# Kernel tuning notes

Hardware: AMD Instinct MI355X
Metric: run time of the kernel (lower is better)

Reference implementation:

```python
import jax, jax.numpy as jnp
import numpy as np

TOP_K = 2
LB_WEIGHT = 0.01


def _ln(x, g, b, eps=1e-5):
    m = x.mean(-1, keepdims=True)
    v = ((x - m) ** 2).mean(-1, keepdims=True)
    return (x - m) * jax.lax.rsqrt(v + eps) * g + b


def setup_inputs() -> dict:
    key = jax.random.key(0)
    ks = iter(jax.random.split(key, 40))
    B, L, D, CT, CB, E, H = 8, 1024, 1024, 768, 64, 8, 1024
    ID = 3 * D           # concat(id, content_proj, collab_proj)
    GH = max(ID // 2, 128)  # 1536, router gate hidden

    def rn(shape, s=0.02):
        return jax.random.normal(next(ks), shape, jnp.float32) * s

    return {
        "id_emb": rn((B, L, D), 1.0),
        "content_emb": rn((B, L, CT), 1.0),
        "collab_emb": rn((B, L, CB), 1.0),
        "ln_ct_g": jnp.ones(CT), "ln_ct_b": jnp.zeros(CT),
        "ln_cb_g": jnp.ones(CB), "ln_cb_b": jnp.zeros(CB),
        "Wc": rn((CT, D)), "bc": jnp.zeros(D),
        "Wcb": rn((CB, D)), "bcb": jnp.zeros(D),
        "Wg1": rn((ID, GH)), "bg1": jnp.zeros(GH),
        "lng_g": jnp.ones(GH), "lng_b": jnp.zeros(GH),
        "Wg2": rn((GH, GH // 2)), "bg2": jnp.zeros(GH // 2),
        "Wg3": rn((GH // 2, E)), "bg3": jnp.zeros(E),
        "We1": rn((E, ID, H)), "be1": jnp.zeros((E, H)),
        "lne1_g": jnp.ones((E, H)), "lne1_b": jnp.zeros((E, H)),
        "We2": rn((E, H, H // 2)), "be2": jnp.zeros((E, H // 2)),
        "We3": rn((E, H // 2, H // 4)), "be3": jnp.zeros((E, H // 4)),
        "lne3_g": jnp.ones((E, H // 4)), "lne3_b": jnp.zeros((E, H // 4)),
        "Wout": rn((H // 4, D)), "bout": jnp.zeros(D),
        "alpha": jnp.full((1,), 0.1, jnp.float32),
    }


def reference(id_emb, content_emb, collab_emb, ln_ct_g, ln_ct_b, ln_cb_g, ln_cb_b,
              Wc, bc, Wcb, bcb, Wg1, bg1, lng_g, lng_b, Wg2, bg2, Wg3, bg3,
              We1, be1, lne1_g, lne1_b, We2, be2, We3, be3, lne3_g, lne3_b,
              Wout, bout, alpha):
    # --- input normalization + projection to d_model (eval mode: no noise/dropout) ---
    ct = _ln(content_emb, ln_ct_g, ln_ct_b) @ Wc + bc        # (B,L,D)
    cb = _ln(collab_emb, ln_cb_g, ln_cb_b) @ Wcb + bcb       # (B,L,D)
    x = jnp.concatenate([id_emb, ct, cb], axis=-1)           # (B,L,3D)

    # --- router: gate MLP -> softmax -> top-k -> renormalize ---
    g = jax.nn.relu(_ln(x @ Wg1 + bg1, lng_g, lng_b))
    g = jax.nn.relu(g @ Wg2 + bg2)
    probs = jax.nn.softmax(g @ Wg3 + bg3, axis=-1)           # (B,L,E)
    topv, topi = jax.lax.top_k(probs, TOP_K)                 # (B,L,K)
    w = topv / (topv.sum(-1, keepdims=True) + 1e-8)

    # --- experts (dense over E, then gather selected) ---
    h = jax.nn.relu(_ln(jnp.einsum('bld,edh->bleh', x, We1) + be1, lne1_g, lne1_b))
    h = jax.nn.relu(jnp.einsum('bleh,ehm->blem', h, We2) + be2)
    eo = _ln(jnp.einsum('blem,emo->bleo', h, We3) + be3, lne3_g, lne3_b)  # (B,L,E,H/4)
    sel = jnp.take_along_axis(eo, topi[..., None], axis=2)   # (B,L,K,H/4)
    comb = (sel * w[..., None]).sum(axis=2)                  # (B,L,H/4)

    # --- output projection + learnable-alpha residual ---
    fused = id_emb + alpha * (comb @ Wout + bout)            # (B,L,D)

    # --- load balancing loss (importance + entropy terms) ---
    E = probs.shape[-1]
    num_tokens = probs.shape[0] * probs.shape[1]
    counts = jnp.sum(jax.nn.one_hot(topi, E, dtype=jnp.float32), axis=(0, 1, 2))
    f = counts / num_tokens
    P = probs.mean(axis=(0, 1))
    importance = E * (f * P).sum()
    ent = -(P * jnp.log(P + 1e-8)).sum()
    max_ent = jnp.log(jnp.asarray(E, jnp.float32))
    lb_loss = (importance + (max_ent - ent) / max_ent) * LB_WEIGHT
    return fused, lb_loss
```

## Files before the change

kernel.cpp:

```cpp
#include <hip/hip_runtime.h>
#include <hip/hip_bf16.h>

using u16 = unsigned short;
typedef float f32x4 __attribute__((ext_vector_type(4)));
typedef short short8 __attribute__((ext_vector_type(8)));
typedef unsigned short ushort8 __attribute__((ext_vector_type(8)));

typedef __attribute__((address_space(1))) const unsigned int gu32;
typedef __attribute__((address_space(3))) unsigned int lu32;

__device__ __forceinline__ float b2f(u16 u) {
  unsigned v = ((unsigned)u) << 16;
  float f;
  __builtin_memcpy(&f, &v, 4);
  return f;
}
__device__ __forceinline__ u16 f2b(float f) {
  unsigned u;
  __builtin_memcpy(&u, &f, 4);
  unsigned r = (u + 0x7fffu + ((u >> 16) & 1u)) >> 16;
  return (u16)r;
}
__device__ __forceinline__ float ldv(float x) { return x; }
__device__ __forceinline__ float ldv(u16 x) { return b2f(x); }

__device__ __forceinline__ void gl_lds16(const void* g, void* l) {
  __builtin_amdgcn_global_load_lds((gu32*)g, (lu32*)l, 16, 0, 0);
}

template <int D, bool RELU, bool PEREXP, typename TIN>
__global__ void ln_rows(const TIN* __restrict__ in, u16* __restrict__ out,
                        const float* __restrict__ gamma, const float* __restrict__ beta,
                        const int* __restrict__ pairExp, const int* __restrict__ total) {
  constexpr int T = (D >= 256) ? 256 : 64;
  constexpr int VPT = D / T;
  int row = blockIdx.x;
  if constexpr (PEREXP) {
    if (row >= *total) return;
  }
  int t = threadIdx.x;
  const TIN* r = in + (size_t)row * D;
  float vals[VPT];
  float s = 0.f, ss = 0.f;
#pragma unroll
  for (int i = 0; i < VPT; ++i) {
    float v = ldv(r[t + i * T]);
    vals[i] = v;
    s += v;
    ss += v * v;
  }
#pragma unroll
  for (int m = 1; m < 64; m <<= 1) {
    s += __shfl_xor(s, m);
    ss += __shfl_xor(ss, m);
  }
  if constexpr (T == 256) {
    __shared__ float red[8];
    int wave = t >> 6, lane = t & 63;
    if (lane == 0) { red[wave] = s; red[4 + wave] = ss; }
    __syncthreads();
    s = red[0] + red[1] + red[2] + red[3];
    ss = red[4] + red[5] + red[6] + red[7];
  }
  float mean = s / (float)D;
  float var = ss / (float)D - mean * mean;
  var = fmaxf(var, 0.f);
  float rstd = 1.f / sqrtf(var + 1e-5f);
  const float* g = gamma;
  const float* b = beta;
  if constexpr (PEREXP) {
    int e = pairExp[row];
    g += (size_t)e * D;
    b += (size_t)e * D;
  }
  u16* o = out + (size_t)row * D;
#pragma unroll
  for (int i = 0; i < VPT; ++i) {
    int idx = t + i * T;
    float v = (vals[i] - mean) * rstd * g[idx] + b[idx];
    if constexpr (RELU) v = fmaxf(v, 0.f);
    o[idx] = f2b(v);
  }
}

struct PackDesc {
  const float* src;
  u16* dst;
  int K, M, tx, tilesPerMat, base;
};
struct PackTable { PackDesc d[8]; int total; };

__global__ void prepack_all(PackTable tab) {
  int bid = blockIdx.x;
  int w = 0;
#pragma unroll
  for (int i = 1; i < 8; ++i)
    if (bid >= tab.d[i].base) w = i;
  PackDesc pd = tab.d[w];
  int local = bid - pd.base;
  int z = local / pd.tilesPerMat;
  int tl = local % pd.tilesPerMat;
  int m0 = (tl % pd.tx) * 64, k0 = (tl / pd.tx) * 64;
  size_t zo = (size_t)z * pd.K * pd.M;
  const float* ip = pd.src + zo;
  u16* op = pd.dst + zo;

  __shared__ u16 tile[64 * 65];
  int t = threadIdx.x;
#pragma unroll
  for (int h = 0; h < 4; ++h) {
    int u = t + h * 256;
    int kr = u >> 4, mc = (u & 15) * 4;
    f32x4 v = *(const f32x4*)(ip + (size_t)(k0 + kr) * pd.M + m0 + mc);
#pragma unroll
    for (int i = 0; i < 4; ++i) tile[kr * 65 + mc + i] = f2b(v[i]);
  }
  __syncthreads();
#pragma unroll
  for (int h = 0; h < 2; ++h) {
    int u = t + h * 256;
    int mr = u >> 3, kc = (u & 7) * 8;
    ushort8 v;
#pragma unroll
    for (int i = 0; i < 8; ++i) v[i] = tile[(kc + i) * 65 + mr];
    *(ushort8*)(op + (size_t)(m0 + mr) * pd.K + k0 + kc) = v;
  }
}

__global__ void copy_id3(const float* __restrict__ id, u16* __restrict__ xb3) {
  size_t i = ((size_t)blockIdx.x * 256 + threadIdx.x) * 8;
  size_t t = i >> 10, d = i & 1023;
  f32x4 a = *(const f32x4*)(id + i);
  f32x4 b = *(const f32x4*)(id + i + 4);
  ushort8 v;
#pragma unroll
  for (int j = 0; j < 4; ++j) { v[j] = f2b(a[j]); v[j + 4] = f2b(b[j]); }
  *(ushort8*)(xb3 + t * 3072 + d) = v;
}

#define BM 128
#define BN 128
#define BKK 64

template <int EPI, bool EXPERT, bool GATHER>
__global__ __launch_bounds__(256, 3)
void gemm_bf(const u16* __restrict__ A, const u16* __restrict__ Bt,
             const float* __restrict__ bias,
             u16* __restrict__ C, float* __restrict__ Cf,
             int K, int lda, int ldc,
             long strideB, int strideBias,
             const int* __restrict__ offA, const int* __restrict__ pairTok,
             const float* __restrict__ resid, const float* __restrict__ alphaPtr) {
  int rowTile = blockIdx.x * BM;
  int colTile = blockIdx.y * BN;
  if constexpr (EXPERT) {
    if (rowTile >= offA[8]) return;
    int e = 0;
    while (rowTile >= offA[e + 1]) ++e;
    Bt += (size_t)e * strideB;
    bias += (size_t)e * strideBias;
  }

  __shared__ u16 As[BM * BKK];
  __shared__ u16 Bs[BN * BKK];

  int t = threadIdx.x;
  int lane = t & 63;
  int wv = t >> 6;
  int wr = wv >> 1, wc = wv & 1;
  int l15 = lane & 15, l4 = lane >> 4;

  int rowInLane = lane >> 3;
  int colLane = (lane & 7) * 8;
  const u16* aSrc[4];
  const u16* bSrc[4];
  u16* aDst[4];
  u16* bDst[4];
#pragma unroll
  for (int j = 0; j < 4; ++j) {
    int rr = j * 32 + wv * 8 + rowInLane;
    size_t aRow;
    if constexpr (GATHER) {
      aRow = (size_t)pairTok[rowTile + rr] * lda;
    } else {
      aRow = (size_t)(rowTile + rr) * lda;
    }
    aSrc[j] = A + aRow + colLane;
    bSrc[j] = Bt + (size_t)(colTile + rr) * K + colLane;
    aDst[j] = As + (j * 32 + wv * 8) * BKK;
    bDst[j] = Bs + (j * 32 + wv * 8) * BKK;
  }

  f32x4 zero4 = {0.f, 0.f, 0.f, 0.f};
  f32x4 acc[4][4];
#pragma unroll
  for (int m = 0; m < 4; ++m)
#pragma unroll
    for (int n = 0; n < 4; ++n) acc[m][n] = zero4;

  for (int k0 = 0; k0 < K; k0 += BKK) {
    __syncthreads();
#pragma unroll
    for (int j = 0; j < 4; ++j) gl_lds16(aSrc[j] + k0, aDst[j]);
#pragma unroll
    for (int j = 0; j < 4; ++j) gl_lds16(bSrc[j] + k0, bDst[j]);
    asm volatile("s_waitcnt vmcnt(0)" ::: "memory");
    __syncthreads();
    short8 af[4][2];
#pragma unroll
    for (int m = 0; m < 4; ++m)
#pragma unroll
      for (int ks = 0; ks < 2; ++ks)
        af[m][ks] = *(const short8*)&As[(wr * 64 + m * 16 + l15) * BKK + ks * 32 + l4 * 8];
#pragma unroll
    for (int n = 0; n < 4; ++n) {
      short8 bfr[2];
#pragma unroll
      for (int ks = 0; ks < 2; ++ks)
        bfr[ks] = *(const short8*)&Bs[(wc * 64 + n * 16 + l15) * BKK + ks * 32 + l4 * 8];
#pragma unroll
      for (int m = 0; m < 4; ++m)
#pragma unroll
        for (int ks = 0; ks < 2; ++ks)
          acc[m][n] = __builtin_amdgcn_mfma_f32_16x16x32_bf16(af[m][ks], bfr[ks], acc[m][n], 0, 0, 0);
    }
  }

  float alphaV = 0.f;
  if constexpr (EPI == 2) alphaV = alphaPtr[0];
#pragma unroll
  for (int n = 0; n < 4; ++n) {
    int col = colTile + wc * 64 + n * 16 + l15;
    float bv = bias[col];
#pragma unroll
    for (int m = 0; m < 4; ++m) {
      int r2 = rowTile + wr * 64 + m * 16 + l4 * 4;
#pragma unroll
      for (int j = 0; j < 4; ++j) {
        float v = acc[m][n][j] + bv;
        if constexpr (EPI == 1) v = fmaxf(v, 0.f);
        if constexpr (EPI == 2) {
          Cf[(size_t)(r2 + j) * ldc + col] =
              resid[(size_t)(r2 + j) * ldc + col] + alphaV * v;
        } else {
          C[(size_t)(r2 + j) * ldc + col] = f2b(v);
        }
      }
    }
  }
}

__global__ void router_kernel(const u16* __restrict__ g2, const float* __restrict__ Wg3,
                              const float* __restrict__ bg3, float* __restrict__ probs,
                              int* __restrict__ topi, float* __restrict__ wts) {
  int tok = blockIdx.x * 4 + (threadIdx.x >> 6);
  int lane = threadIdx.x & 63;
  const u16* row = g2 + (size_t)tok * 768;
  float acc[8];
#pragma unroll
  for (int e = 0; e < 8; ++e) acc[e] = 0.f;
  for (int j = lane; j < 768; j += 64) {
    float v = b2f(row[j]);
    f32x4 w0 = *(const f32x4*)(Wg3 + (size_t)j * 8);
    f32x4 w1 = *(const f32x4*)(Wg3 + (size_t)j * 8 + 4);
#pragma unroll
    for (int e = 0; e < 4; ++e) { acc[e] += v * w0[e]; acc[e + 4] += v * w1[e]; }
  }
#pragma unroll
  for (int e = 0; e < 8; ++e) {
#pragma unroll
    for (int m = 1; m < 64; m <<= 1) acc[e] += __shfl_xor(acc[e], m);
  }
  if (lane == 0) {
    float lg[8], mx = -3.4e38f;
#pragma unroll
    for (int e = 0; e < 8; ++e) {
      lg[e] = acc[e] + bg3[e];
      mx = fmaxf(mx, lg[e]);
    }
    float p[8], s = 0.f;
#pragma unroll
    for (int e = 0; e < 8; ++e) {
      p[e] = expf(lg[e] - mx);
      s += p[e];
    }
    float inv = 1.f / s;
#pragma unroll
    for (int e = 0; e < 8; ++e) {
      p[e] *= inv;
      probs[(size_t)tok * 8 + e] = p[e];
    }
    int i0 = 0;
    for (int e = 1; e < 8; ++e)
      if (p[e] > p[i0]) i0 = e;
    int i1 = (i0 == 0) ? 1 : 0;
    for (int e = 0; e < 8; ++e)
      if (e != i0 && p[e] > p[i1]) i1 = e;
    float w0 = p[i0], w1 = p[i1];
    float wsum = w0 + w1 + 1e-8f;
    topi[tok * 2] = i0;
    topi[tok * 2 + 1] = i1;
    wts[tok * 2] = w0 / wsum;
    wts[tok * 2 + 1] = w1 / wsum;
  }
}

__global__ void count_kernel(const int* __restrict__ topi, int* __restrict__ cnt,
                             int* __restrict__ offA, int* __restrict__ cursor) {
  __shared__ int c[8];
  int t = threadIdx.x;
  if (t < 8) c[t] = 0;
  __syncthreads();
  for (int i = t; i < 16384; i += 256) atomicAdd(&c[topi[i]], 1);
  __syncthreads();
  if (t == 0) {
    int off = 0;
    for (int e = 0; e < 8; ++e) {
      cnt[e] = c[e];
      offA[e] = off;
      cursor[e] = off;
      off += (c[e] + 127) & ~127;
    }
    offA[8] = off;
  }
}

__global__ void scatter_kernel(const int* __restrict__ topi, int* __restrict__ cursor,
                               int* __restrict__ pairTok, int* __restrict__ pairExp,
                               int* __restrict__ posOf) {
  int i = blockIdx.x * 256 + threadIdx.x;
  int e = topi[i];
  int pos = atomicAdd(&cursor[e], 1);
  pairTok[pos] = i >> 1;
  pairExp[pos] = e;
  posOf[i] = pos;
}

__global__ void padfill_kernel(const int* __restrict__ cnt, const int* __restrict__ offA,
                               int* __restrict__ pairTok, int* __restrict__ pairExp) {
  int e = blockIdx.x;
  int start = offA[e] + cnt[e];
  int end = offA[e + 1];
  for (int i = start + threadIdx.x; i < end; i += 256) {
    pairTok[i] = 0;
    pairExp[i] = e;
  }
}

__global__ void combine_kernel(const u16* __restrict__ eo, const int* __restrict__ posOf,
                               const float* __restrict__ wts, u16* __restrict__ comb) {
  int t = blockIdx.x, d = threadIdx.x;
  int p0 = posOf[t * 2], p1 = posOf[t * 2 + 1];
  float w0 = wts[t * 2], w1 = wts[t * 2 + 1];
  float v = w0 * b2f(eo[(size_t)p0 * 256 + d]) + w1 * b2f(eo[(size_t)p1 * 256 + d]);
  comb[(size_t)t * 256 + d] = f2b(v);
}

__global__ void lbloss_kernel(const float* __restrict__ probs, const int* __restrict__ cnt,
                              float* __restrict__ outp) {
  __shared__ float red[256];
  int t = threadIdx.x;
  float pl[8];
#pragma unroll
  for (int e = 0; e < 8; ++e) pl[e] = 0.f;
  for (int i = t; i < 8192; i += 256) {
#pragma unroll
    for (int e = 0; e < 8; ++e) pl[e] += probs[(size_t)i * 8 + e];
  }
  float P[8];
  for (int e = 0; e < 8; ++e) {
    red[t] = pl[e];
    __syncthreads();
    for (int s = 128; s > 0; s >>= 1) {
      if (t < s) red[t] += red[t + s];
      __syncthreads();
    }
    P[e] = red[0] / 8192.f;
    __syncthreads();
  }
  if (t == 0) {
    float imp = 0.f, ent = 0.f;
    for (int e = 0; e < 8; ++e) {
      float f = (float)cnt[e] / 8192.f;
      imp += f * P[e];
      ent -= P[e] * logf(P[e] + 1e-8f);
    }
    imp *= 8.f;
    float maxent = logf(8.f);
    outp[0] = (imp + (maxent - ent) / maxent) * 0.01f;
  }
}

extern "C" void kernel_launch(void* const* d_in, const int* in_sizes, int n_in,
                              void* d_out, int out_size, void* d_ws, size_t ws_size,
                              hipStream_t stream) {
  const float* id_emb   = (const float*)d_in[0];
  const float* content  = (const float*)d_in[1];
  const float* collab   = (const float*)d_in[2];
  const float* ln_ct_g  = (const float*)d_in[3];
  const float* ln_ct_b  = (const float*)d_in[4];
  const float* ln_cb_g  = (const float*)d_in[5];
  const float* ln_cb_b  = (const float*)d_in[6];
  const float* Wc       = (const float*)d_in[7];
  const float* bc       = (const float*)d_in[8];
  const float* Wcb      = (const float*)d_in[9];
  const float* bcb      = (const float*)d_in[10];
  const float* Wg1      = (const float*)d_in[11];
  const float* bg1      = (const float*)d_in[12];
  const float* lng_g    = (const float*)d_in[13];
  const float* lng_b    = (const float*)d_in[14];
  const float* Wg2      = (const float*)d_in[15];
  const float* bg2      = (const float*)d_in[16];
  const float* Wg3      = (const float*)d_in[17];
  const float* bg3      = (const float*)d_in[18];
  const float* We1      = (const float*)d_in[19];
  const float* be1      = (const float*)d_in[20];
  const float* lne1_g   = (const float*)d_in[21];
  const float* lne1_b   = (const float*)d_in[22];
  const float* We2      = (const float*)d_in[23];
  const float* be2      = (const float*)d_in[24];
  const float* We3      = (const float*)d_in[25];
  const float* be3      = (const float*)d_in[26];
  const float* lne3_g   = (const float*)d_in[27];
  const float* lne3_b   = (const float*)d_in[28];
  const float* Wout     = (const float*)d_in[29];
  const float* bout     = (const float*)d_in[30];
  const float* alpha    = (const float*)d_in[31];
  (void)in_sizes; (void)n_in; (void)out_size; (void)ws_size;

  float* out = (float*)d_out;
  char* ws = (char*)d_ws;
  size_t o = 0;
  auto AL = [&](size_t bytes) {
    size_t r = o;
    o += (bytes + 255) & ~(size_t)255;
    return r;
  };

  u16* WcT   = (u16*)(ws + AL(1024ull * 768 * 2));
  u16* WcbT  = (u16*)(ws + AL(1024ull * 64 * 2));
  u16* Wg1T  = (u16*)(ws + AL(1536ull * 3072 * 2));
  u16* Wg2T  = (u16*)(ws + AL(768ull * 1536 * 2));
  u16* We1T  = (u16*)(ws + AL(8ull * 1024 * 3072 * 2));
  u16* We2T  = (u16*)(ws + AL(8ull * 512 * 1024 * 2));
  u16* We3T  = (u16*)(ws + AL(8ull * 256 * 512 * 2));
  u16* WoutT = (u16*)(ws + AL(1024ull * 256 * 2));
  u16* xb3   = (u16*)(ws + AL(8192ull * 3072 * 2));
  size_t R1  = AL(17408ull * 1024 * 2);
  u16* ct_norm = (u16*)(ws + R1);
  u16* cb_norm = (u16*)(ws + R1 + 8192ull * 768 * 2);
  u16* g1      = (u16*)(ws + R1);
  u16* h1      = (u16*)(ws + R1);
  size_t R2  = AL(17408ull * 512 * 2);
  u16* g2 = (u16*)(ws + R2);
  u16* h2 = (u16*)(ws + R2);
  u16* eo   = (u16*)(ws + AL(17408ull * 256 * 2));
  u16* comb = (u16*)(ws + AL(8192ull * 256 * 2));
  float* probs = (float*)(ws + AL(8192ull * 8 * 4));
  int* topi    = (int*)(ws + AL(8192ull * 2 * 4));
  float* wts   = (float*)(ws + AL(8192ull * 2 * 4));
  int* posOf   = (int*)(ws + AL(8192ull * 2 * 4));
  int* pairTok = (int*)(ws + AL(17408ull * 4));
  int* pairExp = (int*)(ws + AL(17408ull * 4));
  int* cnt     = (int*)(ws + AL(64));
  int* offA    = (int*)(ws + AL(64));
  int* cursor  = (int*)(ws + AL(64));

  PackTable tab;
  auto mk = [](const float* s, u16* d, int K, int M, int z) {
    PackDesc p;
    p.src = s; p.dst = d; p.K = K; p.M = M;
    p.tx = M / 64; p.tilesPerMat = (M / 64) * (K / 64); p.base = 0;
    return p;
  };
  PackDesc descs[8] = {
      mk(Wc, WcT, 768, 1024, 1),    mk(Wcb, WcbT, 64, 1024, 1),
      mk(Wg1, Wg1T, 3072, 1536, 1), mk(Wg2, Wg2T, 1536, 768, 1),
      mk(We1, We1T, 3072, 1024, 8), mk(We2, We2T, 1024, 512, 8),
      mk(We3, We3T, 512, 256, 8),   mk(Wout, WoutT, 256, 1024, 1)};
  int zcount[8] = {1, 1, 1, 1, 8, 8, 8, 1};
  int base = 0;
  for (int i = 0; i < 8; ++i) {
    descs[i].base = base;
    base += descs[i].tilesPerMat * zcount[i];
  }
  for (int i = 0; i < 8; ++i) tab.d[i] = descs[i];
  tab.total = base;
  prepack_all<<<base, 256, 0, stream>>>(tab);

  ln_rows<768, false, false, float><<<8192, 256, 0, stream>>>(content, ct_norm, ln_ct_g, ln_ct_b, nullptr, nullptr);
  ln_rows<64, false, false, float><<<8192, 64, 0, stream>>>(collab, cb_norm, ln_cb_g, ln_cb_b, nullptr, nullptr);
  copy_id3<<<4096, 256, 0, stream>>>(id_emb, xb3);
  gemm_bf<0, false, false><<<dim3(64, 8), 256, 0, stream>>>(
      ct_norm, WcT, bc, xb3 + 1024, nullptr, 768, 768, 3072,
      0, 0, nullptr, nullptr, nullptr, nullptr);
  gemm_bf<0, false, false><<<dim3(64, 8), 256, 0, stream>>>(
      cb_norm, WcbT, bcb, xb3 + 2048, nullptr, 64, 64, 3072,
      0, 0, nullptr, nullptr, nullptr, nullptr);

  gemm_bf<0, false, false><<<dim3(64, 12), 256, 0, stream>>>(
      xb3, Wg1T, bg1, g1, nullptr, 3072, 3072, 1536,
      0, 0, nullptr, nullptr, nullptr, nullptr);
  ln_rows<1536, true, false, u16><<<8192, 256, 0, stream>>>(g1, g1, lng_g, lng_b, nullptr, nullptr);
  gemm_bf<1, false, false><<<dim3(64, 6), 256, 0, stream>>>(
      g1, Wg2T, bg2, g2, nullptr, 1536, 1536, 768,
      0, 0, nullptr, nullptr, nullptr, nullptr);
  router_kernel<<<2048, 256, 0, stream>>>(g2, Wg3, bg3, probs, topi, wts);

  count_kernel<<<1, 256, 0, stream>>>(topi, cnt, offA, cursor);
  scatter_kernel<<<64, 256, 0, stream>>>(topi, cursor, pairTok, pairExp, posOf);
  padfill_kernel<<<8, 256, 0, stream>>>(cnt, offA, pairTok, pairExp);

  gemm_bf<0, true, true><<<dim3(136, 8), 256, 0, stream>>>(
      xb3, We1T, be1, h1, nullptr, 3072, 3072, 1024,
      3072l * 1024, 1024, offA, pairTok, nullptr, nullptr);
  ln_rows<1024, true, true, u16><<<17408, 256, 0, stream>>>(h1, h1, lne1_g, lne1_b, pairExp, offA + 8);
  gemm_bf<1, true, false><<<dim3(136, 4), 256, 0, stream>>>(
      h1, We2T, be2, h2, nullptr, 1024, 1024, 512,
      512l * 1024, 512, offA, nullptr, nullptr, nullptr);
  gemm_bf<0, true, false><<<dim3(136, 2), 256, 0, stream>>>(
      h2, We3T, be3, eo, nullptr, 512, 512, 256,
      256l * 512, 256, offA, nullptr, nullptr, nullptr);
  ln_rows<256, false, true, u16><<<17408, 256, 0, stream>>>(eo, eo, lne3_g, lne3_b, pairExp, offA + 8);
  combine_kernel<<<8192, 256, 0, stream>>>(eo, posOf, wts, comb);

  gemm_bf<2, false, false><<<dim3(64, 8), 256, 0, stream>>>(
      comb, WoutT, bout, nullptr, out, 256, 256, 1024,
      0, 0, nullptr, nullptr, id_emb, alpha);

  lbloss_kernel<<<1, 256, 0, stream>>>(probs, cnt, out + 8388608);
}
```

Measured before the change: 644.3 us.

## Fuse expert LN into combine, merge scatter/padfill, add XCD swizzle for expert GEMMs

```diff
diff --git a/kernel.cpp b/kernel.cpp
--- a/kernel.cpp
+++ b/kernel.cpp
@@ -83,6 +83,23 @@
   }
 }
 
+__global__ void ln_rows64(const float* __restrict__ in, u16* __restrict__ out,
+                          const float* __restrict__ gamma, const float* __restrict__ beta) {
+  int row = blockIdx.x * 4 + (threadIdx.x >> 6);
+  int lane = threadIdx.x & 63;
+  float v = in[(size_t)row * 64 + lane];
+  float s = v, q = v * v;
+#pragma unroll
+  for (int m = 1; m < 64; m <<= 1) {
+    s += __shfl_xor(s, m);
+    q += __shfl_xor(q, m);
+  }
+  float mean = s / 64.f;
+  float var = fmaxf(q / 64.f - mean * mean, 0.f);
+  float rstd = 1.f / sqrtf(var + 1e-5f);
+  out[(size_t)row * 64 + lane] = f2b((v - mean) * rstd * gamma[lane] + beta[lane]);
+}
+
 struct PackDesc {
   const float* src;
   u16* dst;
@@ -142,7 +159,7 @@
 #define BN 128
 #define BKK 64
 
-template <int EPI, bool EXPERT, bool GATHER>
+template <int EPI, bool EXPERT, bool GATHER, bool SWZ>
 __global__ __launch_bounds__(256, 3)
 void gemm_bf(const u16* __restrict__ A, const u16* __restrict__ Bt,
              const float* __restrict__ bias,
@@ -151,8 +168,20 @@
              long strideB, int strideBias,
              const int* __restrict__ offA, const int* __restrict__ pairTok,
              const float* __restrict__ resid, const float* __restrict__ alphaPtr) {
-  int rowTile = blockIdx.x * BM;
-  int colTile = blockIdx.y * BN;
+  int rowTile, colTile;
+  if constexpr (SWZ) {
+    int gy = gridDim.y;
+    int nwg = gridDim.x * gy;
+    int id = blockIdx.x * gy + blockIdx.y;
+    int q = nwg >> 3, r = nwg & 7;
+    int xcd = id & 7, pos = id >> 3;
+    int nid = (xcd < r) ? (xcd * (q + 1) + pos) : (r * (q + 1) + (xcd - r) * q + pos);
+    rowTile = (nid / gy) * BM;
+    colTile = (nid % gy) * BN;
+  } else {
+    rowTile = blockIdx.x * BM;
+    colTile = blockIdx.y * BN;
+  }
   if constexpr (EXPERT) {
     if (rowTile >= offA[8]) return;
     int e = 0;
@@ -325,35 +354,59 @@
   }
 }
 
-__global__ void scatter_kernel(const int* __restrict__ topi, int* __restrict__ cursor,
-                               int* __restrict__ pairTok, int* __restrict__ pairExp,
-                               int* __restrict__ posOf) {
-  int i = blockIdx.x * 256 + threadIdx.x;
-  int e = topi[i];
-  int pos = atomicAdd(&cursor[e], 1);
-  pairTok[pos] = i >> 1;
-  pairExp[pos] = e;
-  posOf[i] = pos;
-}
-
-__global__ void padfill_kernel(const int* __restrict__ cnt, const int* __restrict__ offA,
-                               int* __restrict__ pairTok, int* __restrict__ pairExp) {
-  int e = blockIdx.x;
-  int start = offA[e] + cnt[e];
-  int end = offA[e + 1];
-  for (int i = start + threadIdx.x; i < end; i += 256) {
-    pairTok[i] = 0;
-    pairExp[i] = e;
-  }
-}
-
-__global__ void combine_kernel(const u16* __restrict__ eo, const int* __restrict__ posOf,
-                               const float* __restrict__ wts, u16* __restrict__ comb) {
+__global__ void scatter_padfill(const int* __restrict__ topi, int* __restrict__ cursor,
+                                const int* __restrict__ cnt, const int* __restrict__ offA,
+                                int* __restrict__ pairTok, int* __restrict__ pairExp,
+                                int* __restrict__ posOf) {
+  if (blockIdx.x < 64) {
+    int i = blockIdx.x * 256 + threadIdx.x;
+    int e = topi[i];
+    int pos = atomicAdd(&cursor[e], 1);
+    pairTok[pos] = i >> 1;
+    pairExp[pos] = e;
+    posOf[i] = pos;
+  } else {
+    int e = blockIdx.x - 64;
+    int start = offA[e] + cnt[e];
+    int end = offA[e + 1];
+    for (int i = start + threadIdx.x; i < end; i += 256) {
+      pairTok[i] = 0;
+      pairExp[i] = e;
+    }
+  }
+}
+
+__global__ void combine_ln(const u16* __restrict__ eo, const int* __restrict__ posOf,
+                           const int* __restrict__ pairExp, const float* __restrict__ wts,
+                           const float* __restrict__ g3, const float* __restrict__ b3,
+                           u16* __restrict__ comb) {
   int t = blockIdx.x, d = threadIdx.x;
   int p0 = posOf[t * 2], p1 = posOf[t * 2 + 1];
   float w0 = wts[t * 2], w1 = wts[t * 2 + 1];
-  float v = w0 * b2f(eo[(size_t)p0 * 256 + d]) + w1 * b2f(eo[(size_t)p1 * 256 + d]);
-  comb[(size_t)t * 256 + d] = f2b(v);
+  int e0 = pairExp[p0], e1 = pairExp[p1];
+  float v0 = b2f(eo[(size_t)p0 * 256 + d]);
+  float v1 = b2f(eo[(size_t)p1 * 256 + d]);
+  float s0 = v0, q0 = v0 * v0, s1 = v1, q1 = v1 * v1;
+#pragma unroll
+  for (int m = 1; m < 64; m <<= 1) {
+    s0 += __shfl_xor(s0, m);
+    q0 += __shfl_xor(q0, m);
+    s1 += __shfl_xor(s1, m);
+    q1 += __shfl_xor(q1, m);
+  }
+  __shared__ float rs[4][4];
+  int wave = d >> 6, lane = d & 63;
+  if (lane == 0) { rs[wave][0] = s0; rs[wave][1] = q0; rs[wave][2] = s1; rs[wave][3] = q1; }
+  __syncthreads();
+  s0 = rs[0][0] + rs[1][0] + rs[2][0] + rs[3][0];
+  q0 = rs[0][1] + rs[1][1] + rs[2][1] + rs[3][1];
+  s1 = rs[0][2] + rs[1][2] + rs[2][2] + rs[3][2];
+  q1 = rs[0][3] + rs[1][3] + rs[2][3] + rs[3][3];
+  float m0 = s0 / 256.f, var0 = fmaxf(q0 / 256.f - m0 * m0, 0.f), r0 = 1.f / sqrtf(var0 + 1e-5f);
+  float m1 = s1 / 256.f, var1 = fmaxf(q1 / 256.f - m1 * m1, 0.f), r1 = 1.f / sqrtf(var1 + 1e-5f);
+  float n0 = (v0 - m0) * r0 * g3[e0 * 256 + d] + b3[e0 * 256 + d];
+  float n1 = (v1 - m1) * r1 * g3[e1 * 256 + d] + b3[e1 * 256 + d];
+  comb[(size_t)t * 256 + d] = f2b(w0 * n0 + w1 * n1);
 }
 
 __global__ void lbloss_kernel(const float* __restrict__ probs, const int* __restrict__ cnt,
@@ -467,17 +520,17 @@
   int* cursor  = (int*)(ws + AL(64));
 
   PackTable tab;
-  auto mk = [](const float* s, u16* d, int K, int M, int z) {
+  auto mk = [](const float* s, u16* d, int K, int M) {
     PackDesc p;
     p.src = s; p.dst = d; p.K = K; p.M = M;
     p.tx = M / 64; p.tilesPerMat = (M / 64) * (K / 64); p.base = 0;
     return p;
   };
   PackDesc descs[8] = {
-      mk(Wc, WcT, 768, 1024, 1),    mk(Wcb, WcbT, 64, 1024, 1),
-      mk(Wg1, Wg1T, 3072, 1536, 1), mk(Wg2, Wg2T, 1536, 768, 1),
-      mk(We1, We1T, 3072, 1024, 8), mk(We2, We2T, 1024, 512, 8),
-      mk(We3, We3T, 512, 256, 8),   mk(Wout, WoutT, 256, 1024, 1)};
+      mk(Wc, WcT, 768, 1024),    mk(Wcb, WcbT, 64, 1024),
+      mk(Wg1, Wg1T, 3072, 1536), mk(Wg2, Wg2T, 1536, 768),
+      mk(We1, We1T, 3072, 1024), mk(We2, We2T, 1024, 512),
+      mk(We3, We3T, 512, 256),   mk(Wout, WoutT, 256, 1024)};
   int zcount[8] = {1, 1, 1, 1, 8, 8, 8, 1};
   int base = 0;
   for (int i = 0; i < 8; ++i) {
@@ -489,42 +542,40 @@
   prepack_all<<<base, 256, 0, stream>>>(tab);
 
   ln_rows<768, false, false, float><<<8192, 256, 0, stream>>>(content, ct_norm, ln_ct_g, ln_ct_b, nullptr, nullptr);
-  ln_rows<64, false, false, float><<<8192, 64, 0, stream>>>(collab, cb_norm, ln_cb_g, ln_cb_b, nullptr, nullptr);
+  ln_rows64<<<2048, 256, 0, stream>>>(collab, cb_norm, ln_cb_g, ln_cb_b);
   copy_id3<<<4096, 256, 0, stream>>>(id_emb, xb3);
-  gemm_bf<0, false, false><<<dim3(64, 8), 256, 0, stream>>>(
+  gemm_bf<0, false, false, false><<<dim3(64, 8), 256, 0, stream>>>(
       ct_norm, WcT, bc, xb3 + 1024, nullptr, 768, 768, 3072,
       0, 0, nullptr, nullptr, nullptr, nullptr);
-  gemm_bf<0, false, false><<<dim3(64, 8), 256, 0, stream>>>(
+  gemm_bf<0, false, false, false><<<dim3(64, 8), 256, 0, stream>>>(
       cb_norm, WcbT, bcb, xb3 + 2048, nullptr, 64, 64, 3072,
       0, 0, nullptr, nullptr, nullptr, nullptr);
 
-  gemm_bf<0, false, false><<<dim3(64, 12), 256, 0, stream>>>(
+  gemm_bf<0, false, false, false><<<dim3(64, 12), 256, 0, stream>>>(
       xb3, Wg1T, bg1, g1, nullptr, 3072, 3072, 1536,
       0, 0, nullptr, nullptr, nullptr, nullptr);
   ln_rows<1536, true, false, u16><<<8192, 256, 0, stream>>>(g1, g1, lng_g, lng_b, nullptr, nullptr);
-  gemm_bf<1, false, false><<<dim3(64, 6), 256, 0, stream>>>(
+  gemm_bf<1, false, false, false><<<dim3(64, 6), 256, 0, stream>>>(
       g1, Wg2T, bg2, g2, nullptr, 1536, 1536, 768,
       0, 0, nullptr, nullptr, nullptr, nullptr);
   router_kernel<<<2048, 256, 0, stream>>>(g2, Wg3, bg3, probs, topi, wts);
 
   count_kernel<<<1, 256, 0, stream>>>(topi, cnt, offA, cursor);
-  scatter_kernel<<<64, 256, 0, stream>>>(topi, cursor, pairTok, pairExp, posOf);
-  padfill_kernel<<<8, 256, 0, stream>>>(cnt, offA, pairTok, pairExp);
-
-  gemm_bf<0, true, true><<<dim3(136, 8), 256, 0, stream>>>(
+  scatter_padfill<<<72, 256, 0, stream>>>(topi, cursor, cnt, offA, pairTok, pairExp, posOf);
+
+  gemm_bf<0, true, true, true><<<dim3(136, 8), 256, 0, stream>>>(
       xb3, We1T, be1, h1, nullptr, 3072, 3072, 1024,
       3072l * 1024, 1024, offA, pairTok, nullptr, nullptr);
   ln_rows<1024, true, true, u16><<<17408, 256, 0, stream>>>(h1, h1, lne1_g, lne1_b, pairExp, offA + 8);
-  gemm_bf<1, true, false><<<dim3(136, 4), 256, 0, stream>>>(
+  gemm_bf<1, true, false, true><<<dim3(136, 4), 256, 0, stream>>>(
       h1, We2T, be2, h2, nullptr, 1024, 1024, 512,
       512l * 1024, 512, offA, nullptr, nullptr, nullptr);
-  gemm_bf<0, true, false><<<dim3(136, 2), 256, 0, stream>>>(
+  gemm_bf<0, true, false, true><<<dim3(136, 2), 256, 0, stream>>>(
       h2, We3T, be3, eo, nullptr, 512, 512, 256,
       256l * 512, 256, offA, nullptr, nullptr, nullptr);
-  ln_rows<256, false, true, u16><<<17408, 256, 0, stream>>>(eo, eo, lne3_g, lne3_b, pairExp, offA + 8);
-  combine_kernel<<<8192, 256, 0, stream>>>(eo, posOf, wts, comb);
-
-  gemm_bf<2, false, false><<<dim3(64, 8), 256, 0, stream>>>(
+  combine_ln<<<8192, 256, 0, stream>>>(eo, posOf, pairExp, wts, lne3_g, lne3_b, comb);
+
+  gemm_bf<2, false, false, false><<<dim3(64, 8), 256, 0, stream>>>(
       comb, WoutT, bout, nullptr, out, 256, 256, 1024,
       0, 0, nullptr, nullptr, id_emb, alpha);
 
```

After: 628.6 us (median of 2 runs). -2.4%, faster.
